# Optimization experiments

Measured on AMD Instinct MI355X. Metric: run time of the kernel, lower is better.

Reference implementation:

```python
import jax, jax.numpy as jnp
import numpy as np

NUM_EMBEDDINGS = 1024
EMBEDDING_DIM = 64
COMMITMENT_COST = 0.25


def setup_inputs() -> dict:
    key = jax.random.key(0)
    k_in, k_w = jax.random.split(key)
    inputs = jax.random.normal(k_in, (32, 64, 32, 32), dtype=jnp.float32)
    # nn.Embedding weight initialized uniform(-1/K, 1/K)
    bound = 1.0 / NUM_EMBEDDINGS
    weight = jax.random.uniform(k_w, (NUM_EMBEDDINGS, EMBEDDING_DIM),
                                dtype=jnp.float32, minval=-bound, maxval=bound)
    return {"inputs": inputs, "weight": weight}


def reference(inputs, weight):
    # Flatten to [N, D] rows in embedding space
    flat = inputs.reshape(-1, EMBEDDING_DIM)  # [N, D]
    distances = (jnp.sum(flat * flat, axis=1, keepdims=True)
                 + jnp.sum(weight * weight, axis=1)
                 - 2.0 * jnp.matmul(flat, weight.T))
    encoding_indices = jnp.argmin(distances, axis=1)  # [N]
    quantized = weight[encoding_indices].reshape(inputs.shape)
    e_latent_loss = jnp.mean((jax.lax.stop_gradient(quantized) - inputs) ** 2)
    q_latent_loss = jnp.mean((quantized - jax.lax.stop_gradient(inputs)) ** 2)
    commitment_loss = COMMITMENT_COST * (q_latent_loss + e_latent_loss)
    # Straight-through estimator
    quantized = inputs + jax.lax.stop_gradient(quantized - inputs)
    return quantized, encoding_indices[:, None], commitment_loss
```

## Files before the change

### kernel.cpp

```cpp
#include <hip/hip_runtime.h>

#define NROWS  32768
#define DIM    64
#define KCODES 1024
#define NELEM  (NROWS * DIM)
#define NBLK_B 512
#define RPB_B  64

typedef float v2f __attribute__((ext_vector_type(2)));

__device__ __forceinline__ float np_sumsq_f4(const float4* __restrict__ p) {
#pragma clang fp contract(off)
  float4 a = p[0], b = p[1];
  float r0 = a.x * a.x, r1 = a.y * a.y, r2 = a.z * a.z, r3 = a.w * a.w;
  float r4 = b.x * b.x, r5 = b.y * b.y, r6 = b.z * b.z, r7 = b.w * b.w;
#pragma unroll
  for (int i = 1; i < 8; ++i) {
    a = p[2 * i]; b = p[2 * i + 1];
    r0 += a.x * a.x; r1 += a.y * a.y; r2 += a.z * a.z; r3 += a.w * a.w;
    r4 += b.x * b.x; r5 += b.y * b.y; r6 += b.z * b.z; r7 += b.w * b.w;
  }
  return ((r0 + r1) + (r2 + r3)) + ((r4 + r5) + (r6 + r7));
}

__global__ __launch_bounds__(256) void vq_prep(const float* __restrict__ x,
                                               const float* __restrict__ w,
                                               float* __restrict__ sxv,
                                               float* __restrict__ se,
                                               double* __restrict__ loss,
                                               unsigned int* __restrict__ cnt) {
  const int t = blockIdx.x * 256 + threadIdx.x;
  if (t == 0) { *loss = 0.0; *cnt = 0u; }
  sxv[t] = np_sumsq_f4((const float4*)(x + (size_t)t * DIM));
  if (t < KCODES) se[t] = np_sumsq_f4((const float4*)(w + (size_t)t * DIM));
}

__global__ __launch_bounds__(256, 2) void vq_dist(const float* __restrict__ x,
                                                  const float* __restrict__ w,
                                                  const float* __restrict__ sxv,
                                                  const float* __restrict__ seg,
                                                  unsigned long long* __restrict__ keys) {
  __shared__ float xs[128 * 64];
  __shared__ float ws[64 * 128];
  const int t = threadIdx.x;
  const int rg = blockIdx.x >> 3;
  const int cc = blockIdx.x & 7;
  const int row0 = rg * 128;
  const int c0 = cc * 128;

  {
    const float4* xg = (const float4*)x + (size_t)row0 * 16;
    const float4* wg = (const float4*)w + (size_t)c0 * 16;
    float4* xs4 = (float4*)xs;
#pragma unroll
    for (int i = 0; i < 8; ++i) {
      const int g = t + 256 * i;
      const int rr = g >> 4, f4 = g & 15;
      xs4[rr * 16 + (f4 ^ (rr & 15))] = xg[g];
      float4 u = wg[g];
      const int k0 = f4 * 4;
      const int clo = rr & 3, chi = rr >> 2;
      ws[(k0 + 0) * 128 + ((chi ^ ((k0 + 0) & 31)) << 2) + clo] = u.x;
      ws[(k0 + 1) * 128 + ((chi ^ ((k0 + 1) & 31)) << 2) + clo] = u.y;
      ws[(k0 + 2) * 128 + ((chi ^ ((k0 + 2) & 31)) << 2) + clo] = u.z;
      ws[(k0 + 3) * 128 + ((chi ^ ((k0 + 3) & 31)) << 2) + clo] = u.w;
    }
  }
  __syncthreads();

  const int m = t & 15, a = t >> 4;
  v2f acc[8][4];
#pragma unroll
  for (int j = 0; j < 8; ++j)
#pragma unroll
    for (int p = 0; p < 4; ++p) acc[j][p] = (v2f){0.f, 0.f};

  const float4* xs4 = (const float4*)xs;
  const float4* ws4 = (const float4*)ws;

#pragma unroll 2
  for (int kb = 0; kb < 16; ++kb) {
    float4 xf[8];
#pragma unroll
    for (int j = 0; j < 8; ++j)
      xf[j] = xs4[(m + 16 * j) * 16 + (kb ^ m)];
    v2f wf[4][4];
#pragma unroll
    for (int kk = 0; kk < 4; ++kk) {
      const int k = kb * 4 + kk, sw = k & 31;
      float4 u0 = ws4[k * 32 + (a ^ sw)];
      float4 u1 = ws4[k * 32 + ((a + 16) ^ sw)];
      wf[kk][0] = (v2f){u0.x, u0.y}; wf[kk][1] = (v2f){u0.z, u0.w};
      wf[kk][2] = (v2f){u1.x, u1.y}; wf[kk][3] = (v2f){u1.z, u1.w};
    }
#pragma unroll
    for (int j = 0; j < 8; ++j) {
#pragma unroll
      for (int p = 0; p < 4; ++p) {
        acc[j][p] += (v2f){xf[j].x, xf[j].x} * wf[0][p];
        acc[j][p] += (v2f){xf[j].y, xf[j].y} * wf[1][p];
        acc[j][p] += (v2f){xf[j].z, xf[j].z} * wf[2][p];
        acc[j][p] += (v2f){xf[j].w, xf[j].w} * wf[3][p];
      }
    }
  }

  unsigned long long bk[8];
#pragma unroll
  for (int j = 0; j < 8; ++j) {
    const float sx = sxv[row0 + m + 16 * j];
    unsigned long long best = ~0ull;
#pragma unroll
    for (int p = 0; p < 4; ++p) {
      const int cb = c0 + 4 * a + ((p < 2) ? 2 * p : 64 + 2 * (p - 2));
      const float d0 = fmaf(-2.0f, acc[j][p].x, sx + seg[cb]);
      const float d1 = fmaf(-2.0f, acc[j][p].y, sx + seg[cb + 1]);
      const unsigned long long k0v =
          ((unsigned long long)__float_as_uint(d0) << 32) | (unsigned int)cb;
      const unsigned long long k1v =
          ((unsigned long long)__float_as_uint(d1) << 32) | (unsigned int)(cb + 1);
      if (k0v < best) best = k0v;
      if (k1v < best) best = k1v;
    }
    bk[j] = best;
  }

  __syncthreads();
  unsigned long long* kred = (unsigned long long*)xs;
#pragma unroll
  for (int j = 0; j < 8; ++j) kred[(m + 16 * j) * 17 + a] = bk[j];
  __syncthreads();
  if (t < 128) {
    unsigned long long mn = kred[t * 17];
#pragma unroll
    for (int q = 1; q < 16; ++q) {
      const unsigned long long kq = kred[t * 17 + q];
      if (kq < mn) mn = kq;
    }
    keys[((size_t)(row0 + t) << 3) | cc] = mn;
  }
}

__global__ __launch_bounds__(256) void vq_out(const float* __restrict__ x,
                                              const float* __restrict__ w,
                                              const unsigned long long* __restrict__ keys,
                                              float* __restrict__ outq,
                                              float* __restrict__ outidx,
                                              double* __restrict__ loss,
                                              unsigned int* __restrict__ cnt,
                                              float* __restrict__ outloss) {
  __shared__ int sidx[RPB_B];
  __shared__ double part[4];
  const int b = blockIdx.x, t = threadIdx.x;

  if (t < RPB_B) {
    const int row = b * RPB_B + t;
    const unsigned long long* kr = keys + ((size_t)row << 3);
    unsigned long long mn = kr[0];
#pragma unroll
    for (int i = 1; i < 8; ++i) { unsigned long long k = kr[i]; if (k < mn) mn = k; }
    const int idx = (int)(unsigned int)(mn & 0xFFFFFFFFull);
    outidx[row] = (float)idx;
    sidx[t] = idx;
  }
  __syncthreads();

  double acc = 0.0;
  const float4* x4 = (const float4*)x;
  float4* o4 = (float4*)outq;
#pragma unroll
  for (int i = 0; i < 4; ++i) {
    const int e = i * 256 + t;
    const int rl = e >> 4;
    const int d4 = e & 15;
    const size_t gofs = ((size_t)b * RPB_B + rl) * 16 + d4;
    float4 xvv = x4[gofs];
    const float4* wr = (const float4*)(w + (size_t)sidx[rl] * DIM);
    float4 wv = wr[d4];
    float tx = wv.x - xvv.x, ty = wv.y - xvv.y;
    float tz = wv.z - xvv.z, tw = wv.w - xvv.w;
    float4 q;
    q.x = xvv.x + tx; q.y = xvv.y + ty;
    q.z = xvv.z + tz; q.w = xvv.w + tw;
    o4[gofs] = q;
    acc += (double)tx * tx + (double)ty * ty + (double)tz * tz + (double)tw * tw;
  }

#pragma unroll
  for (int s = 32; s > 0; s >>= 1) acc += __shfl_down(acc, s, 64);
  if ((t & 63) == 0) part[t >> 6] = acc;
  __syncthreads();
  if (t == 0) {
    atomicAdd(loss, (part[0] + part[1]) + (part[2] + part[3]));
    __threadfence();
    unsigned int old = atomicAdd(cnt, 1u);
    if (old == NBLK_B - 1) {
      double L = atomicAdd(loss, 0.0);
      *outloss = 0.5f * (float)(L / (double)NELEM);
    }
  }
}

extern "C" void kernel_launch(void* const* d_in, const int* in_sizes, int n_in,
                              void* d_out, int out_size, void* d_ws, size_t ws_size,
                              hipStream_t stream) {
  const float* x = (const float*)d_in[0];
  const float* w = (const float*)d_in[1];

  float* outq    = (float*)d_out;
  float* outidx  = outq + NELEM;
  float* outloss = outidx + NROWS;

  char* wsb = (char*)d_ws;
  double* loss = (double*)wsb;
  unsigned int* cnt = (unsigned int*)(wsb + 64);
  float* sxv = (float*)(wsb + 4096);
  float* se  = (float*)(wsb + 4096 + 131072);
  unsigned long long* keys = (unsigned long long*)(wsb + 139264);

  hipLaunchKernelGGL(vq_prep, dim3(128),  dim3(256), 0, stream,
                     x, w, sxv, se, loss, cnt);
  hipLaunchKernelGGL(vq_dist, dim3(2048), dim3(256), 0, stream,
                     x, w, sxv, se, keys);
  hipLaunchKernelGGL(vq_out,  dim3(NBLK_B), dim3(256), 0, stream,
                     x, w, keys, outq, outidx, loss, cnt, outloss);
}
```

Baseline: 143.6 us.

## Restructure distance GEMM microkernel with transposed x tile and inline packed FMA

Reorganizes the vq_dist register tile. Each thread now owns 8 consecutive rows and 8 consecutive codes. X is stored transposed in LDS as row pairs and W row-major with an XOR swizzle. The inner loop uses inline-asm v_pk_fma_f32 with op_sel to broadcast a single W scalar against packed x pairs, which avoids the per-FMA broadcast moves. The aim is fewer LDS reads and VALU instructions per FMA, at the cost of fully unrolled loops and inline asm that may raise register pressure or reorder the fp accumulation.

```diff
diff --git a/kernel.cpp b/kernel.cpp
--- a/kernel.cpp
+++ b/kernel.cpp
@@ -8,6 +8,16 @@
 #define RPB_B  64
 
 typedef float v2f __attribute__((ext_vector_type(2)));
+typedef float v4f __attribute__((ext_vector_type(4)));
+
+__device__ __forceinline__ void pk_fma_lo(v2f& acc, v2f xp, v2f wp) {
+  asm("v_pk_fma_f32 %0, %1, %2, %0 op_sel:[0,0,0] op_sel_hi:[1,0,1]"
+      : "+v"(acc) : "v"(xp), "v"(wp));
+}
+__device__ __forceinline__ void pk_fma_hi(v2f& acc, v2f xp, v2f wp) {
+  asm("v_pk_fma_f32 %0, %1, %2, %0 op_sel:[0,1,0] op_sel_hi:[1,1,1]"
+      : "+v"(acc) : "v"(xp), "v"(wp));
+}
 
 __device__ __forceinline__ float np_sumsq_f4(const float4* __restrict__ p) {
 #pragma clang fp contract(off)
@@ -40,95 +50,110 @@
                                                   const float* __restrict__ sxv,
                                                   const float* __restrict__ seg,
                                                   unsigned long long* __restrict__ keys) {
-  __shared__ float xs[128 * 64];
-  __shared__ float ws[64 * 128];
+  __shared__ float xst[64 * 128];
+  __shared__ float wst[128 * 64];
   const int t = threadIdx.x;
   const int rg = blockIdx.x >> 3;
-  const int cc = blockIdx.x & 7;
+  const int chunk = blockIdx.x & 7;
   const int row0 = rg * 128;
-  const int c0 = cc * 128;
+  const int c0 = chunk * 128;
 
   {
     const float4* xg = (const float4*)x + (size_t)row0 * 16;
     const float4* wg = (const float4*)w + (size_t)c0 * 16;
-    float4* xs4 = (float4*)xs;
+    float4* wst4 = (float4*)wst;
 #pragma unroll
     for (int i = 0; i < 8; ++i) {
       const int g = t + 256 * i;
       const int rr = g >> 4, f4 = g & 15;
-      xs4[rr * 16 + (f4 ^ (rr & 15))] = xg[g];
+      float4 q = xg[g];
+      const int p = rr >> 1, o = rr & 1;
+#pragma unroll
+      for (int j = 0; j < 4; ++j) {
+        const int k = 4 * f4 + j;
+        const int pslot = p ^ ((k & 15) << 2);
+        const float val = (j == 0) ? q.x : (j == 1) ? q.y : (j == 2) ? q.z : q.w;
+        xst[k * 128 + ((pslot << 1) | o)] = val;
+      }
       float4 u = wg[g];
-      const int k0 = f4 * 4;
-      const int clo = rr & 3, chi = rr >> 2;
-      ws[(k0 + 0) * 128 + ((chi ^ ((k0 + 0) & 31)) << 2) + clo] = u.x;
-      ws[(k0 + 1) * 128 + ((chi ^ ((k0 + 1) & 31)) << 2) + clo] = u.y;
-      ws[(k0 + 2) * 128 + ((chi ^ ((k0 + 2) & 31)) << 2) + clo] = u.z;
-      ws[(k0 + 3) * 128 + ((chi ^ ((k0 + 3) & 31)) << 2) + clo] = u.w;
-    }
-  }
-  __syncthreads();
-
-  const int m = t & 15, a = t >> 4;
-  v2f acc[8][4];
-#pragma unroll
-  for (int j = 0; j < 8; ++j)
-#pragma unroll
-    for (int p = 0; p < 4; ++p) acc[j][p] = (v2f){0.f, 0.f};
-
-  const float4* xs4 = (const float4*)xs;
-  const float4* ws4 = (const float4*)ws;
-
-#pragma unroll 2
-  for (int kb = 0; kb < 16; ++kb) {
-    float4 xf[8];
-#pragma unroll
-    for (int j = 0; j < 8; ++j)
-      xf[j] = xs4[(m + 16 * j) * 16 + (kb ^ m)];
-    v2f wf[4][4];
+      wst4[rr * 16 + (f4 ^ ((rr >> 3) & 7))] = u;
+    }
+  }
+  __syncthreads();
+
+  const int C = t & 15;
+  const int R = t >> 4;
+  const int C7 = C & 7;
+
+  v2f acc[4][8];
+#pragma unroll
+  for (int u = 0; u < 4; ++u)
+#pragma unroll
+    for (int oc = 0; oc < 8; ++oc) acc[u][oc] = (v2f){0.f, 0.f};
+
+  const v2f* xs2 = (const v2f*)xst;
+  const v4f* ws4 = (const v4f*)wst;
+  const int wbase = C << 7;
+
+#pragma unroll
+  for (int f4 = 0; f4 < 16; ++f4) {
+    v4f wq[8];
+    const int wo = wbase + (f4 ^ C7);
+#pragma unroll
+    for (int oc = 0; oc < 8; ++oc) wq[oc] = ws4[wo + (oc << 4)];
 #pragma unroll
     for (int kk = 0; kk < 4; ++kk) {
-      const int k = kb * 4 + kk, sw = k & 31;
-      float4 u0 = ws4[k * 32 + (a ^ sw)];
-      float4 u1 = ws4[k * 32 + ((a + 16) ^ sw)];
-      wf[kk][0] = (v2f){u0.x, u0.y}; wf[kk][1] = (v2f){u0.z, u0.w};
-      wf[kk][2] = (v2f){u1.x, u1.y}; wf[kk][3] = (v2f){u1.z, u1.w};
-    }
-#pragma unroll
-    for (int j = 0; j < 8; ++j) {
-#pragma unroll
-      for (int p = 0; p < 4; ++p) {
-        acc[j][p] += (v2f){xf[j].x, xf[j].x} * wf[0][p];
-        acc[j][p] += (v2f){xf[j].y, xf[j].y} * wf[1][p];
-        acc[j][p] += (v2f){xf[j].z, xf[j].z} * wf[2][p];
-        acc[j][p] += (v2f){xf[j].w, xf[j].w} * wf[3][p];
+      const int k = 4 * f4 + kk;
+      const int xb = (k << 6) + ((R ^ (k & 15)) << 2);
+      v2f xp0 = xs2[xb + 0];
+      v2f xp1 = xs2[xb + 1];
+      v2f xp2 = xs2[xb + 2];
+      v2f xp3 = xs2[xb + 3];
+#pragma unroll
+      for (int oc = 0; oc < 8; ++oc) {
+        v2f wp = (kk < 2) ? __builtin_shufflevector(wq[oc], wq[oc], 0, 1)
+                          : __builtin_shufflevector(wq[oc], wq[oc], 2, 3);
+        if ((kk & 1) == 0) {
+          pk_fma_lo(acc[0][oc], xp0, wp); pk_fma_lo(acc[1][oc], xp1, wp);
+          pk_fma_lo(acc[2][oc], xp2, wp); pk_fma_lo(acc[3][oc], xp3, wp);
+        } else {
+          pk_fma_hi(acc[0][oc], xp0, wp); pk_fma_hi(acc[1][oc], xp1, wp);
+          pk_fma_hi(acc[2][oc], xp2, wp); pk_fma_hi(acc[3][oc], xp3, wp);
+        }
       }
     }
   }
 
+  float sxr[8], sev[8];
+#pragma unroll
+  for (int j = 0; j < 8; ++j) sxr[j] = sxv[row0 + 8 * R + j];
+#pragma unroll
+  for (int oc = 0; oc < 8; ++oc) sev[oc] = seg[c0 + 8 * C + oc];
+
   unsigned long long bk[8];
 #pragma unroll
-  for (int j = 0; j < 8; ++j) {
-    const float sx = sxv[row0 + m + 16 * j];
-    unsigned long long best = ~0ull;
-#pragma unroll
-    for (int p = 0; p < 4; ++p) {
-      const int cb = c0 + 4 * a + ((p < 2) ? 2 * p : 64 + 2 * (p - 2));
-      const float d0 = fmaf(-2.0f, acc[j][p].x, sx + seg[cb]);
-      const float d1 = fmaf(-2.0f, acc[j][p].y, sx + seg[cb + 1]);
-      const unsigned long long k0v =
-          ((unsigned long long)__float_as_uint(d0) << 32) | (unsigned int)cb;
-      const unsigned long long k1v =
-          ((unsigned long long)__float_as_uint(d1) << 32) | (unsigned int)(cb + 1);
-      if (k0v < best) best = k0v;
-      if (k1v < best) best = k1v;
-    }
-    bk[j] = best;
-  }
-
-  __syncthreads();
-  unsigned long long* kred = (unsigned long long*)xs;
-#pragma unroll
-  for (int j = 0; j < 8; ++j) kred[(m + 16 * j) * 17 + a] = bk[j];
+  for (int u = 0; u < 4; ++u) {
+#pragma unroll
+    for (int h = 0; h < 2; ++h) {
+      const float sx = sxr[2 * u + h];
+      unsigned long long best = ~0ull;
+#pragma unroll
+      for (int oc = 0; oc < 8; ++oc) {
+        const float dot = h ? acc[u][oc].y : acc[u][oc].x;
+        const float d = fmaf(-2.0f, dot, sx + sev[oc]);
+        const unsigned long long key =
+            ((unsigned long long)__float_as_uint(d) << 32) |
+            (unsigned int)(c0 + 8 * C + oc);
+        if (key < best) best = key;
+      }
+      bk[2 * u + h] = best;
+    }
+  }
+
+  __syncthreads();
+  unsigned long long* kred = (unsigned long long*)xst;
+#pragma unroll
+  for (int j = 0; j < 8; ++j) kred[(8 * R + j) * 17 + C] = bk[j];
   __syncthreads();
   if (t < 128) {
     unsigned long long mn = kred[t * 17];
@@ -137,7 +162,7 @@
       const unsigned long long kq = kred[t * 17 + q];
       if (kq < mn) mn = kq;
     }
-    keys[((size_t)(row0 + t) << 3) | cc] = mn;
+    keys[((size_t)(row0 + t) << 3) | chunk] = mn;
   }
 }
 
```

New measurement: 147.8 us. 1.03x slower.
